# Performance work log

Hardware: AMD Instinct MI355X
Metric: run time of the kernel (lower is better)

## Reference

```python
import jax, jax.numpy as jnp
import numpy as np

B, SQ, SK, D = 8, 4096, 4096, 256  # batch, query len, key len, feature dim (query_dim=key_dim=value_dim=output_dim=256)


def setup_inputs() -> dict:
    key = jax.random.key(0)
    ks = jax.random.split(key, 9)
    s = 1.0 / np.sqrt(D)  # torch Linear default init scale (uniform bound); use for realistic magnitudes
    return {
        "query": jax.random.normal(ks[0], (B, SQ, D), dtype=jnp.float32),
        "keys": jax.random.normal(ks[1], (B, SK, D), dtype=jnp.float32),
        "values": jax.random.normal(ks[2], (B, SK, D), dtype=jnp.float32),
        "Wq": jax.random.uniform(ks[3], (D, D), jnp.float32, -s, s),
        "bq": jax.random.uniform(ks[4], (D,), jnp.float32, -s, s),
        "Wk": jax.random.uniform(ks[5], (D, D), jnp.float32, -s, s),
        "bk": jax.random.uniform(ks[6], (D,), jnp.float32, -s, s),
        "Wv": jax.random.uniform(ks[7], (D, D), jnp.float32, -s, s),
        "bv": jax.random.uniform(ks[8], (D,), jnp.float32, -s, s),
    }


def reference(query, keys, values, Wq, bq, Wk, bk, Wv, bv):
    # Linear projections (torch Linear: x @ W^T + b)
    q = query @ Wq.T + bq            # [B, SQ, D]
    k = keys @ Wk.T + bk             # [B, SK, D]
    v = values @ Wv.T + bv           # [B, SK, D]
    # Unscaled dot-product attention, exactly as in the source (no 1/sqrt(d))
    scores = jnp.einsum("bqd,bkd->bqk", q, k)   # [B, SQ, SK]
    attn = jax.nn.softmax(scores, axis=-1)
    context = jnp.einsum("bqk,bkd->bqd", attn, v)  # [B, SQ, D]
    return context
```

## Files before the change

### kernel.cpp

```cpp
#include <hip/hip_runtime.h>
#include <hip/hip_bf16.h>
#include <math.h>

#define BATCH 8
#define SQL 4096
#define SKL 4096
#define DIM 256
#define KVB 64
#define NIT (SKL / KVB)

typedef __attribute__((ext_vector_type(8))) short short8;
typedef __attribute__((ext_vector_type(4))) float f32x4;
typedef __attribute__((ext_vector_type(4))) float floatx4;

typedef __attribute__((address_space(3))) unsigned int lds_uint;
typedef __attribute__((address_space(1))) unsigned int glob_uint;

__device__ __forceinline__ void gl_lds16(const void* g, void* l) {
  __builtin_amdgcn_global_load_lds((const glob_uint*)g, (lds_uint*)l, 16, 0, 0);
}

__device__ __forceinline__ short f2bf(float f) {
  union { float f; unsigned u; } x; x.f = f;
  unsigned r = x.u + 0x7fffu + ((x.u >> 16) & 1u);
  return (short)(r >> 16);
}

__device__ __forceinline__ int swz(int row) { return (row & 7) << 4; }

__device__ __forceinline__ float dpp_max16(float v) {
  float t;
  t = __int_as_float(__builtin_amdgcn_mov_dpp(__float_as_int(v), 0xB1, 0xF, 0xF, true));
  v = fmaxf(v, t);
  t = __int_as_float(__builtin_amdgcn_mov_dpp(__float_as_int(v), 0x4E, 0xF, 0xF, true));
  v = fmaxf(v, t);
  t = __int_as_float(__builtin_amdgcn_mov_dpp(__float_as_int(v), 0x124, 0xF, 0xF, true));
  v = fmaxf(v, t);
  t = __int_as_float(__builtin_amdgcn_mov_dpp(__float_as_int(v), 0x128, 0xF, 0xF, true));
  v = fmaxf(v, t);
  return v;
}

__global__ __launch_bounds__(256) void wcvt_kernel(
    const float* __restrict__ W0, const float* __restrict__ W1,
    const float* __restrict__ W2, short* __restrict__ out)
{
  const int m = blockIdx.x >> 5;
  const int i = ((blockIdx.x & 31) * 256 + threadIdx.x) * 8;
  const float* W = (m == 0) ? W0 : ((m == 1) ? W1 : W2);
  floatx4 a = *(const floatx4*)(W + i);
  floatx4 c = *(const floatx4*)(W + i + 4);
  short8 v;
  #pragma unroll
  for (int j = 0; j < 4; ++j) { v[j] = f2bf(a[j]); v[j+4] = f2bf(c[j]); }
  *(short8*)(out + (size_t)m * DIM * DIM + i) = v;
}

__global__ __launch_bounds__(256) void proj_kernel(
    const float* __restrict__ X, const short* __restrict__ Wb,
    const float* __restrict__ bias, short* __restrict__ out)
{
  const int lane = threadIdx.x & 63;
  const int wave = threadIdx.x >> 6;
  const int lr = lane & 15, hi = lane >> 4;
  const int m0 = blockIdx.x * 32;
  const int n0 = wave * 64;

  f32x4 acc0[4] = {(f32x4)0.f,(f32x4)0.f,(f32x4)0.f,(f32x4)0.f};
  f32x4 acc1[4] = {(f32x4)0.f,(f32x4)0.f,(f32x4)0.f,(f32x4)0.f};
  const float* xr0 = X + (size_t)(m0 + lr) * DIM;
  const float* xr1 = X + (size_t)(m0 + 16 + lr) * DIM;

  #pragma unroll
  for (int kk = 0; kk < 8; ++kk) {
    const int k8 = kk * 32 + hi * 8;
    floatx4 xa = *(const floatx4*)(xr0 + k8);
    floatx4 xb = *(const floatx4*)(xr0 + k8 + 4);
    floatx4 ya = *(const floatx4*)(xr1 + k8);
    floatx4 yb = *(const floatx4*)(xr1 + k8 + 4);
    short8 a0, a1;
    #pragma unroll
    for (int j = 0; j < 4; ++j) {
      a0[j] = f2bf(xa[j]); a0[j+4] = f2bf(xb[j]);
      a1[j] = f2bf(ya[j]); a1[j+4] = f2bf(yb[j]);
    }
    #pragma unroll
    for (int nb = 0; nb < 4; ++nb) {
      short8 bfr = *(const short8*)(Wb + (size_t)(n0 + nb*16 + lr) * DIM + k8);
      acc0[nb] = __builtin_amdgcn_mfma_f32_16x16x32_bf16(a0, bfr, acc0[nb], 0, 0, 0);
      acc1[nb] = __builtin_amdgcn_mfma_f32_16x16x32_bf16(a1, bfr, acc1[nb], 0, 0, 0);
    }
  }
  #pragma unroll
  for (int nb = 0; nb < 4; ++nb) {
    const int n = n0 + nb*16 + lr;
    const float bv = bias[n];
    #pragma unroll
    for (int r = 0; r < 4; ++r) {
      out[(size_t)(m0 + hi*4 + r) * DIM + n]      = f2bf(acc0[nb][r] + bv);
      out[(size_t)(m0 + 16 + hi*4 + r) * DIM + n] = f2bf(acc1[nb][r] + bv);
    }
  }
}

__global__ __launch_bounds__(256) void projV_kernel(
    const float* __restrict__ X, const short* __restrict__ Wb,
    const float* __restrict__ bias, short* __restrict__ outT)
{
  __shared__ short tile[32][264];
  const int lane = threadIdx.x & 63;
  const int wave = threadIdx.x >> 6;
  const int lr = lane & 15, hi = lane >> 4;
  const int m0 = blockIdx.x * 32;
  const int n0 = wave * 64;

  f32x4 acc0[4] = {(f32x4)0.f,(f32x4)0.f,(f32x4)0.f,(f32x4)0.f};
  f32x4 acc1[4] = {(f32x4)0.f,(f32x4)0.f,(f32x4)0.f,(f32x4)0.f};
  const float* xr0 = X + (size_t)(m0 + lr) * DIM;
  const float* xr1 = X + (size_t)(m0 + 16 + lr) * DIM;

  #pragma unroll
  for (int kk = 0; kk < 8; ++kk) {
    const int k8 = kk * 32 + hi * 8;
    floatx4 xa = *(const floatx4*)(xr0 + k8);
    floatx4 xb = *(const floatx4*)(xr0 + k8 + 4);
    floatx4 ya = *(const floatx4*)(xr1 + k8);
    floatx4 yb = *(const floatx4*)(xr1 + k8 + 4);
    short8 a0, a1;
    #pragma unroll
    for (int j = 0; j < 4; ++j) {
      a0[j] = f2bf(xa[j]); a0[j+4] = f2bf(xb[j]);
      a1[j] = f2bf(ya[j]); a1[j+4] = f2bf(yb[j]);
    }
    #pragma unroll
    for (int nb = 0; nb < 4; ++nb) {
      short8 bfr = *(const short8*)(Wb + (size_t)(n0 + nb*16 + lr) * DIM + k8);
      acc0[nb] = __builtin_amdgcn_mfma_f32_16x16x32_bf16(a0, bfr, acc0[nb], 0, 0, 0);
      acc1[nb] = __builtin_amdgcn_mfma_f32_16x16x32_bf16(a1, bfr, acc1[nb], 0, 0, 0);
    }
  }
  #pragma unroll
  for (int nb = 0; nb < 4; ++nb) {
    const int n = n0 + nb*16 + lr;
    const float bv = bias[n];
    #pragma unroll
    for (int r = 0; r < 4; ++r) {
      tile[hi*4 + r][n]      = f2bf(acc0[nb][r] + bv);
      tile[16 + hi*4 + r][n] = f2bf(acc1[nb][r] + bv);
    }
  }
  __syncthreads();
  const int t = threadIdx.x;
  short8 v0, v1, v2, v3;
  #pragma unroll
  for (int k = 0; k < 8; ++k) {
    v0[k] = tile[k][t]; v1[k] = tile[k+8][t];
    v2[k] = tile[k+16][t]; v3[k] = tile[k+24][t];
  }
  const int b  = m0 >> 12;
  const int k0 = m0 & (SKL - 1);
  short* p = outT + (size_t)b * DIM * SKL + (size_t)t * SKL + k0;
  *(short8*)(p)      = v0;
  *(short8*)(p + 8)  = v1;
  *(short8*)(p + 16) = v2;
  *(short8*)(p + 24) = v3;
}

__global__ __launch_bounds__(512, 1) void attn_kernel(
    const short* __restrict__ Qb, const short* __restrict__ Kb,
    const short* __restrict__ VtG, float* __restrict__ out)
{
  __shared__ alignas(16) short Kt[2][64][256];
  __shared__ alignas(16) short Vt[2][256][64];
  __shared__ alignas(16) short Pl[8][16][72];

  const int tid  = threadIdx.x;
  const int lane = tid & 63;
  const int wave = tid >> 6;
  const int lr = lane & 15, hi = lane >> 4;

  const int b     = blockIdx.x & 7;
  const int qtile = blockIdx.x >> 3;
  const int q0w   = qtile * 128 + wave * 16;

  const short* Qp = Qb  + ((size_t)b * SQL + q0w) * DIM;
  const short* Kp = Kb  + (size_t)b * SKL * DIM;
  const short* Vp = VtG + (size_t)b * DIM * SKL;

  short8 qf[8];
  #pragma unroll
  for (int kk = 0; kk < 8; ++kk)
    qf[kk] = *(const short8*)(Qp + (size_t)lr * DIM + kk*32 + hi*8);

  f32x4 o[16];
  #pragma unroll
  for (int i = 0; i < 16; ++i) o[i] = (f32x4)0.f;
  float mr[4]   = {-3.0e38f,-3.0e38f,-3.0e38f,-3.0e38f};
  float lacc[4] = {0.f,0.f,0.f,0.f};

  auto stage = [&](int buf, int kv) {
    #pragma unroll
    for (int i = 0; i < 4; ++i) {
      const int row0 = wave*8 + i*2;
      const int row  = row0 + (lane >> 5);
      const int colb = ((lane & 31) * 16) ^ swz(row);
      gl_lds16((const char*)(Kp + (size_t)(kv + row) * DIM) + colb, (void*)&Kt[buf][row0][0]);
    }
    #pragma unroll
    for (int i = 0; i < 4; ++i) {
      const int d0 = wave*32 + i*8;
      const int d  = d0 + (lane >> 3);
      const int colb = ((lane & 7) * 16) ^ swz(d);
      gl_lds16((const char*)(Vp + (size_t)d * SKL + kv) + colb, (void*)&Vt[buf][d0][0]);
    }
  };

  stage(0, 0);
  __syncthreads();
  int cur = 0;

  const char* plw = (const char*)&Pl[wave][0][0];

  for (int it = 0; it < NIT; ++it) {
    if (it + 1 < NIT) stage(cur ^ 1, (it + 1) * KVB);

    const char* ktb = (const char*)&Kt[cur][0][0];
    f32x4 s[4];
    #pragma unroll
    for (int ks = 0; ks < 4; ++ks) s[ks] = (f32x4)0.f;
    __builtin_amdgcn_s_setprio(1);
    #pragma unroll
    for (int kk = 0; kk < 8; ++kk) {
      #pragma unroll
      for (int ks = 0; ks < 4; ++ks) {
        const int row = ks*16 + lr;
        short8 kf = *(const short8*)(ktb + row*512 + (((kk*64) + hi*16) ^ swz(row)));
        s[ks] = __builtin_amdgcn_mfma_f32_16x16x32_bf16(qf[kk], kf, s[ks], 0, 0, 0);
      }
    }
    __builtin_amdgcn_s_setprio(0);

    #pragma unroll
    for (int r = 0; r < 4; ++r) {
      float mx = dpp_max16(fmaxf(fmaxf(s[0][r], s[1][r]), fmaxf(s[2][r], s[3][r])));
      if (mx > mr[r]) {
        const float sc = __expf(mr[r] - mx);
        mr[r] = mx;
        lacc[r] *= sc;
        #pragma unroll
        for (int dt = 0; dt < 16; ++dt) o[dt][r] *= sc;
      }
      const int row = hi*4 + r;
      #pragma unroll
      for (int ks = 0; ks < 4; ++ks) {
        const float p = __expf(s[ks][r] - mr[r]);
        lacc[r] += p;
        *(short*)(plw + row*144 + 2*(ks*16 + lr)) = f2bf(p);
      }
    }

    const char* vtb = (const char*)&Vt[cur][0][0];
    short8 pa[2];
    #pragma unroll
    for (int kh = 0; kh < 2; ++kh)
      pa[kh] = *(const short8*)(plw + lr*144 + kh*64 + hi*16);
    __builtin_amdgcn_s_setprio(1);
    #pragma unroll
    for (int dt = 0; dt < 16; ++dt) {
      #pragma unroll
      for (int kh = 0; kh < 2; ++kh) {
        const int d = dt*16 + lr;
        short8 vf = *(const short8*)(vtb + d*128 + ((kh*64 + hi*16) ^ swz(d)));
        o[dt] = __builtin_amdgcn_mfma_f32_16x16x32_bf16(pa[kh], vf, o[dt], 0, 0, 0);
      }
    }
    __builtin_amdgcn_s_setprio(0);

    __syncthreads();
    cur ^= 1;
  }

  float lsum[4];
  #pragma unroll
  for (int r = 0; r < 4; ++r) lsum[r] = lacc[r];
  #pragma unroll
  for (int off = 8; off >= 1; off >>= 1)
    #pragma unroll
    for (int r = 0; r < 4; ++r)
      lsum[r] += __shfl_xor(lsum[r], off, 64);

  float* op = out + ((size_t)b * SQL + q0w) * DIM;
  #pragma unroll
  for (int r = 0; r < 4; ++r) {
    const float inv = 1.0f / lsum[r];
    #pragma unroll
    for (int dt = 0; dt < 16; ++dt)
      op[(size_t)(hi*4 + r) * DIM + dt*16 + lr] = o[dt][r] * inv;
  }
}

extern "C" void kernel_launch(void* const* d_in, const int* in_sizes, int n_in,
                              void* d_out, int out_size, void* d_ws, size_t ws_size,
                              hipStream_t stream) {
  const float* query  = (const float*)d_in[0];
  const float* keys   = (const float*)d_in[1];
  const float* values = (const float*)d_in[2];
  const float* Wq = (const float*)d_in[3];
  const float* bq = (const float*)d_in[4];
  const float* Wk = (const float*)d_in[5];
  const float* bk = (const float*)d_in[6];
  const float* Wv = (const float*)d_in[7];
  const float* bv = (const float*)d_in[8];
  float* out = (float*)d_out;

  const size_t elems = (size_t)BATCH * SQL * DIM;
  short* Qb  = (short*)d_ws;
  short* Kb  = Qb + elems;
  short* VtT = Kb + elems;

  const size_t wbytes    = (size_t)3 * DIM * DIM * sizeof(short);
  const size_t need_base = 3 * elems * sizeof(short) + wbytes;
  short* Wb;
  if (ws_size >= need_base) Wb = VtT + elems;
  else Wb = (short*)((char*)d_out + (size_t)out_size * sizeof(float) - wbytes);
  short* Wqb = Wb;
  short* Wkb = Wb + DIM * DIM;
  short* Wvb = Wb + 2 * DIM * DIM;

  dim3 blk(256, 1, 1);
  dim3 blk512(512, 1, 1);
  wcvt_kernel <<<dim3(96, 1, 1),            blk, 0, stream>>>(Wq, Wk, Wv, Wb);
  proj_kernel <<<dim3(BATCH*SQL/32, 1, 1),  blk, 0, stream>>>(query,  Wqb, bq, Qb);
  proj_kernel <<<dim3(BATCH*SKL/32, 1, 1),  blk, 0, stream>>>(keys,   Wkb, bk, Kb);
  projV_kernel<<<dim3(BATCH*SKL/32, 1, 1),  blk, 0, stream>>>(values, Wvb, bv, VtT);
  attn_kernel <<<dim3(BATCH*SQL/128, 1, 1), blk512, 0, stream>>>(Qb, Kb, VtT, out);
}
```

Before: 310.8 us.

## Split PV matmul across waves by query pairs and feature halves, allow two blocks per CU

The P·V stage is rebuilt so each wave computes a 32-query by 128-feature output tile instead of 16 queries by 256 features. Probabilities and rescale factors go through shared LDS, guarded by an extra barrier each iteration. Each V fragment read from LDS now feeds two MFMAs, and the output accumulator is halved so launch bounds can ask for two blocks per CU. The cost is an added __syncthreads per KV step plus LDS traffic for the scale factors and row sums.

```diff
diff --git a/kernel.cpp b/kernel.cpp
--- a/kernel.cpp
+++ b/kernel.cpp
@@ -166,13 +166,15 @@
   *(short8*)(p + 24) = v3;
 }
 
-__global__ __launch_bounds__(512, 1) void attn_kernel(
+__global__ __launch_bounds__(512, 2) void attn_kernel(
     const short* __restrict__ Qb, const short* __restrict__ Kb,
     const short* __restrict__ VtG, float* __restrict__ out)
 {
   __shared__ alignas(16) short Kt[2][64][256];
   __shared__ alignas(16) short Vt[2][256][64];
-  __shared__ alignas(16) short Pl[8][16][72];
+  __shared__ alignas(16) short Pl[128][64];
+  __shared__ float scs[128];
+  __shared__ float lshare[128];
 
   const int tid  = threadIdx.x;
   const int lane = tid & 63;
@@ -181,9 +183,13 @@
 
   const int b     = blockIdx.x & 7;
   const int qtile = blockIdx.x >> 3;
-  const int q0w   = qtile * 128 + wave * 16;
-
-  const short* Qp = Qb  + ((size_t)b * SQL + q0w) * DIM;
+  const int q0b   = qtile * 128;
+
+  const int qk_q0 = wave * 16;
+  const int pv_q0 = (wave & 3) * 32;
+  const int d0    = (wave >> 2) * 128;
+
+  const short* Qp = Qb  + ((size_t)b * SQL + q0b + qk_q0) * DIM;
   const short* Kp = Kb  + (size_t)b * SKL * DIM;
   const short* Vp = VtG + (size_t)b * DIM * SKL;
 
@@ -192,9 +198,9 @@
   for (int kk = 0; kk < 8; ++kk)
     qf[kk] = *(const short8*)(Qp + (size_t)lr * DIM + kk*32 + hi*8);
 
-  f32x4 o[16];
-  #pragma unroll
-  for (int i = 0; i < 16; ++i) o[i] = (f32x4)0.f;
+  f32x4 o0[8], o1[8];
+  #pragma unroll
+  for (int i = 0; i < 8; ++i) { o0[i] = (f32x4)0.f; o1[i] = (f32x4)0.f; }
   float mr[4]   = {-3.0e38f,-3.0e38f,-3.0e38f,-3.0e38f};
   float lacc[4] = {0.f,0.f,0.f,0.f};
 
@@ -208,10 +214,10 @@
     }
     #pragma unroll
     for (int i = 0; i < 4; ++i) {
-      const int d0 = wave*32 + i*8;
-      const int d  = d0 + (lane >> 3);
+      const int dd0 = wave*32 + i*8;
+      const int d   = dd0 + (lane >> 3);
       const int colb = ((lane & 7) * 16) ^ swz(d);
-      gl_lds16((const char*)(Vp + (size_t)d * SKL + kv) + colb, (void*)&Vt[buf][d0][0]);
+      gl_lds16((const char*)(Vp + (size_t)d * SKL + kv) + colb, (void*)&Vt[buf][dd0][0]);
     }
   };
 
@@ -219,7 +225,7 @@
   __syncthreads();
   int cur = 0;
 
-  const char* plw = (const char*)&Pl[wave][0][0];
+  const char* plB = (const char*)&Pl[0][0];
 
   for (int it = 0; it < NIT; ++it) {
     if (it + 1 < NIT) stage(cur ^ 1, (it + 1) * KVB);
@@ -243,35 +249,55 @@
     #pragma unroll
     for (int r = 0; r < 4; ++r) {
       float mx = dpp_max16(fmaxf(fmaxf(s[0][r], s[1][r]), fmaxf(s[2][r], s[3][r])));
+      float sc = 1.0f;
       if (mx > mr[r]) {
-        const float sc = __expf(mr[r] - mx);
+        sc = __expf(mr[r] - mx);
         mr[r] = mx;
         lacc[r] *= sc;
-        #pragma unroll
-        for (int dt = 0; dt < 16; ++dt) o[dt][r] *= sc;
-      }
-      const int row = hi*4 + r;
+      }
+      const int row = qk_q0 + hi*4 + r;
+      if (lr == 0) scs[row] = sc;
       #pragma unroll
       for (int ks = 0; ks < 4; ++ks) {
         const float p = __expf(s[ks][r] - mr[r]);
         lacc[r] += p;
-        *(short*)(plw + row*144 + 2*(ks*16 + lr)) = f2bf(p);
-      }
-    }
+        *(short*)(plB + row*128 + ((2*(ks*16 + lr)) ^ swz(row))) = f2bf(p);
+      }
+    }
+
+    __syncthreads();
+
+    float sc0[4], sc1[4];
+    #pragma unroll
+    for (int r = 0; r < 4; ++r) {
+      sc0[r] = scs[pv_q0 + hi*4 + r];
+      sc1[r] = scs[pv_q0 + 16 + hi*4 + r];
+    }
+    #pragma unroll
+    for (int dt = 0; dt < 8; ++dt)
+      #pragma unroll
+      for (int r = 0; r < 4; ++r) {
+        o0[dt][r] *= sc0[r];
+        o1[dt][r] *= sc1[r];
+      }
 
     const char* vtb = (const char*)&Vt[cur][0][0];
-    short8 pa[2];
-    #pragma unroll
-    for (int kh = 0; kh < 2; ++kh)
-      pa[kh] = *(const short8*)(plw + lr*144 + kh*64 + hi*16);
+    short8 pa0[2], pa1[2];
+    #pragma unroll
+    for (int kh = 0; kh < 2; ++kh) {
+      const int rowA = pv_q0 + lr, rowB = pv_q0 + 16 + lr;
+      pa0[kh] = *(const short8*)(plB + rowA*128 + ((kh*64 + hi*16) ^ swz(rowA)));
+      pa1[kh] = *(const short8*)(plB + rowB*128 + ((kh*64 + hi*16) ^ swz(rowB)));
+    }
     __builtin_amdgcn_s_setprio(1);
     #pragma unroll
-    for (int dt = 0; dt < 16; ++dt) {
+    for (int dt = 0; dt < 8; ++dt) {
       #pragma unroll
       for (int kh = 0; kh < 2; ++kh) {
-        const int d = dt*16 + lr;
+        const int d = d0 + dt*16 + lr;
         short8 vf = *(const short8*)(vtb + d*128 + ((kh*64 + hi*16) ^ swz(d)));
-        o[dt] = __builtin_amdgcn_mfma_f32_16x16x32_bf16(pa[kh], vf, o[dt], 0, 0, 0);
+        o0[dt] = __builtin_amdgcn_mfma_f32_16x16x32_bf16(pa0[kh], vf, o0[dt], 0, 0, 0);
+        o1[dt] = __builtin_amdgcn_mfma_f32_16x16x32_bf16(pa1[kh], vf, o1[dt], 0, 0, 0);
       }
     }
     __builtin_amdgcn_s_setprio(0);
@@ -288,14 +314,22 @@
     #pragma unroll
     for (int r = 0; r < 4; ++r)
       lsum[r] += __shfl_xor(lsum[r], off, 64);
-
-  float* op = out + ((size_t)b * SQL + q0w) * DIM;
+  if (lr == 0)
+    #pragma unroll
+    for (int r = 0; r < 4; ++r)
+      lshare[qk_q0 + hi*4 + r] = lsum[r];
+  __syncthreads();
+
+  float* op = out + ((size_t)b * SQL + q0b + pv_q0) * DIM + d0;
   #pragma unroll
   for (int r = 0; r < 4; ++r) {
-    const float inv = 1.0f / lsum[r];
-    #pragma unroll
-    for (int dt = 0; dt < 16; ++dt)
-      op[(size_t)(hi*4 + r) * DIM + dt*16 + lr] = o[dt][r] * inv;
+    const float i0 = 1.0f / lshare[pv_q0 + hi*4 + r];
+    const float i1 = 1.0f / lshare[pv_q0 + 16 + hi*4 + r];
+    #pragma unroll
+    for (int dt = 0; dt < 8; ++dt) {
+      op[(size_t)(hi*4 + r) * DIM + dt*16 + lr]      = o0[dt][r] * i0;
+      op[(size_t)(16 + hi*4 + r) * DIM + dt*16 + lr] = o1[dt][r] * i1;
+    }
   }
 }
 
@@ -329,9 +363,9 @@
 
   dim3 blk(256, 1, 1);
   dim3 blk512(512, 1, 1);
-  wcvt_kernel <<<dim3(96, 1, 1),            blk, 0, stream>>>(Wq, Wk, Wv, Wb);
-  proj_kernel <<<dim3(BATCH*SQL/32, 1, 1),  blk, 0, stream>>>(query,  Wqb, bq, Qb);
-  proj_kernel <<<dim3(BATCH*SKL/32, 1, 1),  blk, 0, stream>>>(keys,   Wkb, bk, Kb);
-  projV_kernel<<<dim3(BATCH*SKL/32, 1, 1),  blk, 0, stream>>>(values, Wvb, bv, VtT);
-  attn_kernel <<<dim3(BATCH*SQL/128, 1, 1), blk512, 0, stream>>>(Qb, Kb, VtT, out);
-}
+  wcvt_kernel <<<dim3(96, 1, 1),           blk, 0, stream>>>(Wq, Wk, Wv, Wb);
+  proj_kernel <<<dim3(BATCH*SQL/32, 1, 1), blk, 0, stream>>>(query,  Wqb, bq, Qb);
+  proj_kernel <<<dim3(BATCH*SKL/32, 1, 1), blk, 0, stream>>>(keys,   Wkb, bk, Kb);
+  projV_kernel<<<dim3(BATCH*SKL/32, 1, 1), blk, 0, stream>>>(values, Wvb, bv, VtT);
+  attn_kernel <<<dim3(256, 1, 1), blk512, 0, stream>>>(Qb, Kb, VtT, out);
+}
```

Result: slower. 322.6 us (+3.8%).
